# Optimization experiments

Measured on AMD Instinct MI355X. Metric: run time of the kernel, lower is better.

## Reference

```python
import jax, jax.numpy as jnp
import numpy as np

N = 30000      # input points
M = 7500       # sampled queries = floor(N * ratio), ratio=0.25
K = 16         # neighbors per query
D_X = 64       # input feature dim
D_REL = 64     # point_pos_nn output dim
D_F = D_X + D_REL  # fij_hat dim = 128


def setup_inputs() -> dict:
    key = jax.random.key(0)
    ks = jax.random.split(key, 6)
    x = jax.random.normal(ks[0], (N, D_X), jnp.float32)
    pos = jax.random.normal(ks[1], (N, 3), jnp.float32)
    idx = jax.random.randint(ks[2], (M,), 0, N)
    W_pos = jax.random.normal(ks[3], (10, D_REL), jnp.float32) / jnp.sqrt(10.0)
    b_pos = jnp.zeros((D_REL,), jnp.float32)
    W_att = jax.random.normal(ks[4], (D_F, D_F), jnp.float32) / jnp.sqrt(float(D_F))
    b_att = jnp.zeros((D_F,), jnp.float32)
    W_glob = jax.random.normal(ks[5], (D_F, D_F), jnp.float32) / jnp.sqrt(float(D_F))
    b_glob = jnp.zeros((D_F,), jnp.float32)
    return {"x": x, "pos": pos, "idx": idx, "W_pos": W_pos, "b_pos": b_pos,
            "W_att": W_att, "b_att": b_att, "W_glob": W_glob, "b_glob": b_glob}


def reference(x, pos, idx, W_pos, b_pos, W_att, b_att, W_glob, b_glob):
    # --- KNN: brute-force squared distances from sampled queries to all points ---
    pos_q = pos[idx]                                         # [M, 3]
    d2 = ((pos_q * pos_q).sum(-1)[:, None]
          + (pos * pos).sum(-1)[None, :]
          - 2.0 * pos_q @ pos.T)                             # [M, N]
    _, nbr = jax.lax.top_k(-d2, K)                           # [M, K] neighbor indices

    # --- Local Spatial Encoding (message) ---
    pos_j = pos[nbr]                                         # [M, K, 3]
    pos_i = jnp.broadcast_to(pos_q[:, None, :], pos_j.shape) # [M, K, 3]
    vij = pos_i - pos_j                                      # [M, K, 3]
    dij = jnp.linalg.norm(vij, axis=-1, keepdims=True)       # [M, K, 1]
    rel = jnp.concatenate([pos_i, pos_j, vij, dij], axis=-1) # [M, K, 10]
    rij = jax.nn.relu(rel @ W_pos + b_pos)                   # [M, K, D_REL]

    # --- Attentive pooling ---
    fij = jnp.concatenate([x[nbr], rij], axis=-1)            # [M, K, D_F]
    g = fij @ W_att + b_att                                  # [M, K, D_F]
    s = jax.nn.softmax(g, axis=-1)                           # softmax over feature dim
    aggr = jnp.mean(s * fij, axis=1)                         # mean over K neighbors -> [M, D_F]

    # --- global_nn (update) ---
    return jax.nn.relu(aggr @ W_glob + b_glob)               # [M, D_F]
```

## Files before the change

### kernel.cpp

```cpp
#include <hip/hip_runtime.h>
#include <stdint.h>

#define KQ     8
#define KNB    16
#define CAPC   256
#define CAPG   512
#define NCHUNK 4

typedef short short8 __attribute__((ext_vector_type(8)));
typedef float floatx4 __attribute__((ext_vector_type(4)));
typedef float floatx2 __attribute__((ext_vector_type(2)));

__device__ __forceinline__ unsigned short f2bf(float x) {
  union { float f; uint32_t u; } v; v.f = x;
  uint32_t u = v.u + 0x7FFFu + ((v.u >> 16) & 1u);
  return (unsigned short)(u >> 16);
}
__device__ __forceinline__ float bf2f(unsigned short b) {
  return __uint_as_float(((uint32_t)b) << 16);
}
__device__ __forceinline__ float rfl(float v) {
  return __int_as_float(__builtin_amdgcn_readfirstlane(__float_as_int(v)));
}

static __device__ __forceinline__ floatx2 fma2(floatx2 a, floatx2 b, floatx2 c) {
#if __has_builtin(__builtin_elementwise_fma)
  return __builtin_elementwise_fma(a, b, c);
#else
  floatx2 r; r[0] = fmaf(a[0], b[0], c[0]); r[1] = fmaf(a[1], b[1], c[1]);
  return r;
#endif
}
static __device__ __forceinline__ floatx2 min2(floatx2 a, floatx2 b) {
#if __has_builtin(__builtin_elementwise_min)
  return __builtin_elementwise_min(a, b);
#else
  floatx2 r; r[0] = fminf(a[0], b[0]); r[1] = fminf(a[1], b[1]);
  return r;
#endif
}
static __device__ __forceinline__ floatx2 sp2(float v) {
  floatx2 r; r[0] = v; r[1] = v; return r;
}

__global__ void prep_kernel(const float* __restrict__ pos,
                            const float* __restrict__ W_att,
                            float4* __restrict__ pos4,
                            float* __restrict__ pospk,
                            unsigned short* __restrict__ Wt,
                            int* __restrict__ cnt_g, int N, int Npad2, int M) {
  int id = blockIdx.x * 256 + threadIdx.x;
  if (id < Npad2) {
    int j = id;
    float px = 0.f, py = 0.f, pz = 0.f, pp = 3.0e38f;
    if (j < N) {
      px = pos[3 * j]; py = pos[3 * j + 1]; pz = pos[3 * j + 2];
      pp = fmaf(px, px, fmaf(py, py, pz * pz));
      pos4[j] = make_float4(px, py, pz, pp);
    }
    int pair = j >> 1, h = j & 1;
    float* dst = pospk + (size_t)pair * 8;
    dst[0 + h] = px; dst[2 + h] = py; dst[4 + h] = pz; dst[6 + h] = pp;
  } else if (id < Npad2 + 128 * 128) {
    int t = id - Npad2;
    int c = t >> 7, f = t & 127;
    Wt[f * 128 + c] = f2bf(W_att[t]);
  } else if (id < Npad2 + 128 * 128 + M) {
    cnt_g[id - Npad2 - 128 * 128] = 0;
  }
}

__global__ __launch_bounds__(256) void knn_kernel(
    const float4* __restrict__ pos4, const float4* __restrict__ pospk4,
    const int* __restrict__ idx, uint32_t* __restrict__ cand_g,
    int* __restrict__ cnt_g, int Npad2, int M) {
  __shared__ uint32_t cand[KQ][CAPC];
  __shared__ int cnt[KQ];
  __shared__ float gmin[KQ][16];
  __shared__ float tau_s[KQ];

  const int tid = threadIdx.x;
  const int wid = tid >> 6, lane = tid & 63;
  const int qg = blockIdx.x >> 2, chunk = blockIdx.x & 3;
  const int q0 = qg * KQ;
  const int iters = Npad2 >> 11;
  const int pbase = chunk * (Npad2 >> 3);
  const int jbase = chunk * (Npad2 >> 2);

  float sx[KQ], sy[KQ], sz[KQ];
#pragma unroll
  for (int qi = 0; qi < KQ; ++qi) {
    int m = q0 + qi; if (m >= M) m = M - 1;
    float4 qp = pos4[idx[m]];
    sx[qi] = rfl(-2.f * qp.x); sy[qi] = rfl(-2.f * qp.y);
    sz[qi] = rfl(-2.f * qp.z);
  }
  if (tid < KQ) cnt[tid] = 0;

  floatx2 tmn[KQ];
#pragma unroll
  for (int qi = 0; qi < KQ; ++qi) tmn[qi] = sp2(3.4e38f);
  {
    int pg = (pbase + tid) * 2;
    float4 a = pospk4[pg], b = pospk4[pg + 1];
    for (int it = 0; it < iters; ++it) {
      float4 an = a, bn = b;
      if (it + 1 < iters) {
        int pgn = (pbase + (it + 1) * 256 + tid) * 2;
        an = pospk4[pgn]; bn = pospk4[pgn + 1];
      }
      floatx2 X, Y, Z, W;
      X[0] = a.x; X[1] = a.y; Y[0] = a.z; Y[1] = a.w;
      Z[0] = b.x; Z[1] = b.y; W[0] = b.z; W[1] = b.w;
#pragma unroll
      for (int qi = 0; qi < KQ; ++qi) {
        floatx2 t = fma2(sp2(sx[qi]), X,
                         fma2(sp2(sy[qi]), Y, fma2(sp2(sz[qi]), Z, W)));
        tmn[qi] = min2(tmn[qi], t);
      }
      a = an; b = bn;
    }
  }
#pragma unroll
  for (int qi = 0; qi < KQ; ++qi) {
    float v = fminf(tmn[qi][0], tmn[qi][1]);
    v = fminf(v, __shfl_xor(v, 1));
    v = fminf(v, __shfl_xor(v, 2));
    v = fminf(v, __shfl_xor(v, 4));
    v = fminf(v, __shfl_xor(v, 8));
    if ((tid & 15) == 0) gmin[qi][tid >> 4] = v;
  }
  __syncthreads();
  if (tid < KQ) {
    float t = gmin[tid][0];
#pragma unroll
    for (int g = 1; g < 16; ++g) t = fmaxf(t, gmin[tid][g]);
    tau_s[tid] = t + fabsf(t) * 1e-6f + 1e-7f;
  }
  __syncthreads();
  float tau[KQ];
#pragma unroll
  for (int qi = 0; qi < KQ; ++qi) tau[qi] = rfl(tau_s[qi]);

  {
    int pg = (pbase + tid) * 2;
    float4 a = pospk4[pg], b = pospk4[pg + 1];
    for (int it = 0; it < iters; ++it) {
      float4 an = a, bn = b;
      if (it + 1 < iters) {
        int pgn = (pbase + (it + 1) * 256 + tid) * 2;
        an = pospk4[pgn]; bn = pospk4[pgn + 1];
      }
      floatx2 X, Y, Z, W;
      X[0] = a.x; X[1] = a.y; Y[0] = a.z; Y[1] = a.w;
      Z[0] = b.x; Z[1] = b.y; W[0] = b.z; W[1] = b.w;
      const int j0 = jbase + it * 512 + tid * 2;
#pragma unroll
      for (int qi = 0; qi < KQ; ++qi) {
        floatx2 t = fma2(sp2(sx[qi]), X,
                         fma2(sp2(sy[qi]), Y, fma2(sp2(sz[qi]), Z, W)));
        if (fminf(t[0], t[1]) <= tau[qi]) {
          if (t[0] <= tau[qi]) {
            int sl = atomicAdd(&cnt[qi], 1);
            if (sl < CAPC) cand[qi][sl] = (uint32_t)j0;
          }
          if (t[1] <= tau[qi]) {
            int sl = atomicAdd(&cnt[qi], 1);
            if (sl < CAPC) cand[qi][sl] = (uint32_t)(j0 + 1);
          }
        }
      }
      a = an; b = bn;
    }
  }
  __syncthreads();

#pragma unroll
  for (int i = 0; i < 2; ++i) {
    int qi = wid * 2 + i;
    int m = q0 + qi;
    if (m < M) {
      int nc = cnt[qi]; if (nc > CAPC) nc = CAPC;
      int base = 0;
      if (lane == 0) base = atomicAdd(&cnt_g[m], nc);
      base = __shfl(base, 0);
      for (int s = lane; s < nc; s += 64) {
        int p = base + s;
        if (p < CAPG) cand_g[(size_t)m * CAPG + p] = cand[qi][s];
      }
    }
  }
}

__global__ __launch_bounds__(256) void merge_kernel(
    const float4* __restrict__ pos4, const int* __restrict__ idx,
    const uint32_t* __restrict__ cand_g, const int* __restrict__ cnt_g,
    int* __restrict__ nbr, int M) {
  const int tid = threadIdx.x;
  const int lane = tid & 63;
  const int m = blockIdx.x * 4 + (tid >> 6);
  if (m >= M) return;

  float4 qp = pos4[idx[m]];
  int nc = cnt_g[m]; if (nc > CAPG) nc = CAPG;

  unsigned long long c[CAPG / 64];
#pragma unroll
  for (int ch = 0; ch < CAPG / 64; ++ch) {
    c[ch] = ~0ull;
    int s = ch * 64 + lane;
    if (s < nc) {
      uint32_t j = cand_g[(size_t)m * CAPG + s];
      float4 pj = pos4[j];
      float dot = fmaf(qp.x, pj.x, fmaf(qp.y, pj.y, qp.z * pj.z));
      float tt  = fmaf(-2.f, dot, pj.w);
      float d2  = fmaxf(qp.w + tt, 0.f);
      c[ch] = ((unsigned long long)__float_as_uint(d2) << 32) | j;
    }
  }
#pragma unroll
  for (int r = 0; r < KNB; ++r) {
    unsigned long long mn = c[0];
#pragma unroll
    for (int ch = 1; ch < CAPG / 64; ++ch) mn = (c[ch] < mn) ? c[ch] : mn;
#pragma unroll
    for (int off = 1; off < 64; off <<= 1) {
      unsigned long long o = __shfl_xor(mn, off);
      mn = (o < mn) ? o : mn;
    }
    if (lane == 0) nbr[m * KNB + r] = (int)(uint32_t)mn;
#pragma unroll
    for (int ch = 0; ch < CAPG / 64; ++ch)
      if (c[ch] == mn) c[ch] = ~0ull;
  }
}

__global__ __launch_bounds__(256) void mid_kernel(
    const float* __restrict__ x, const float4* __restrict__ pos4,
    const int* __restrict__ idx, const float* __restrict__ W_pos,
    const float* __restrict__ b_pos, const unsigned short* __restrict__ Wt,
    const float* __restrict__ b_att, const int* __restrict__ nbr,
    float* __restrict__ aggr, int M) {
  __shared__ __align__(16) unsigned short fijb[8][16][136];
  __shared__ int nbr_s[128];
  __shared__ float4 qpos_s[8];

  const int tid = threadIdx.x;
  const int wid = tid >> 6, lane = tid & 63;
  const int col = lane & 15, quad = lane >> 4;
  const int b = blockIdx.x;

  if (tid < 128) {
    int mq = b * 8 + (tid >> 4); if (mq >= M) mq = M - 1;
    nbr_s[tid] = nbr[mq * 16 + (tid & 15)];
  }
  if (tid < 8) {
    int mq = b * 8 + tid; if (mq >= M) mq = M - 1;
    qpos_s[tid] = pos4[idx[mq]];
  }
  float wp[10];
#pragma unroll
  for (int t = 0; t < 10; ++t) wp[t] = W_pos[t * 64 + lane];
  float bp = b_pos[lane];
  __syncthreads();

  {
    int rr = tid >> 1, h = tid & 1;
    int jn = nbr_s[rr];
    const float4* src = (const float4*)(x + (size_t)jn * 64) + h * 8;
    short8* dst = (short8*)&fijb[rr >> 4][rr & 15][h * 32];
#pragma unroll
    for (int i = 0; i < 4; ++i) {
      float4 u = src[2 * i], v = src[2 * i + 1];
      short8 w;
      w[0] = (short)f2bf(u.x); w[1] = (short)f2bf(u.y);
      w[2] = (short)f2bf(u.z); w[3] = (short)f2bf(u.w);
      w[4] = (short)f2bf(v.x); w[5] = (short)f2bf(v.y);
      w[6] = (short)f2bf(v.z); w[7] = (short)f2bf(v.w);
      dst[i] = w;
    }
  }
#pragma unroll
  for (int qi = 0; qi < 2; ++qi) {
    int q = wid * 2 + qi;
    float4 qp = qpos_s[q];
#pragma unroll 4
    for (int k = 0; k < 16; ++k) {
      int jn = nbr_s[q * 16 + k];
      float4 pj = pos4[jn];
      float vx = qp.x - pj.x, vy = qp.y - pj.y, vz = qp.z - pj.z;
      float dd = sqrtf(fmaf(vx, vx, fmaf(vy, vy, vz * vz)));
      float r = bp;
      r = fmaf(qp.x, wp[0], r); r = fmaf(qp.y, wp[1], r); r = fmaf(qp.z, wp[2], r);
      r = fmaf(pj.x, wp[3], r); r = fmaf(pj.y, wp[4], r); r = fmaf(pj.z, wp[5], r);
      r = fmaf(vx, wp[6], r);  r = fmaf(vy, wp[7], r);  r = fmaf(vz, wp[8], r);
      r = fmaf(dd, wp[9], r);
      r = fmaxf(r, 0.f);
      fijb[q][k][64 + lane] = f2bf(r);
    }
  }
  __syncthreads();

#pragma unroll 1
  for (int qi = 0; qi < 2; ++qi) {
    int q = wid * 2 + qi;
    int mq = b * 8 + q;

    short8 af[4];
#pragma unroll
    for (int cs = 0; cs < 4; ++cs)
      af[cs] = *(const short8*)&fijb[q][col][cs * 32 + quad * 8];

    floatx4 acc[8];
#pragma unroll
    for (int ft = 0; ft < 8; ++ft) {
      float bav = b_att[ft * 16 + col];
      floatx4 a = {bav, bav, bav, bav};
#pragma unroll
      for (int cs = 0; cs < 4; ++cs) {
        short8 bfrag =
            *(const short8*)&Wt[(ft * 16 + col) * 128 + cs * 32 + quad * 8];
        a = __builtin_amdgcn_mfma_f32_16x16x32_bf16(af[cs], bfrag, a, 0, 0, 0);
      }
      acc[ft] = a;
    }

    float rowmax[4], rowinv[4];
#pragma unroll
    for (int r = 0; r < 4; ++r) {
      float mx = acc[0][r];
#pragma unroll
      for (int ft = 1; ft < 8; ++ft) mx = fmaxf(mx, acc[ft][r]);
      mx = fmaxf(mx, __shfl_xor(mx, 1));
      mx = fmaxf(mx, __shfl_xor(mx, 2));
      mx = fmaxf(mx, __shfl_xor(mx, 4));
      mx = fmaxf(mx, __shfl_xor(mx, 8));
      float sm = 0.f;
#pragma unroll
      for (int ft = 0; ft < 8; ++ft) sm += __expf(acc[ft][r] - mx);
      sm += __shfl_xor(sm, 1);
      sm += __shfl_xor(sm, 2);
      sm += __shfl_xor(sm, 4);
      sm += __shfl_xor(sm, 8);
      rowmax[r] = mx;
      rowinv[r] = 1.0f / sm;
    }

#pragma unroll
    for (int ft = 0; ft < 8; ++ft) {
      float ap = 0.f;
#pragma unroll
      for (int r = 0; r < 4; ++r) {
        float s = __expf(acc[ft][r] - rowmax[r]) * rowinv[r];
        float fv = bf2f(fijb[q][quad * 4 + r][ft * 16 + col]);
        ap = fmaf(s, fv, ap);
      }
      ap += __shfl_xor(ap, 16);
      ap += __shfl_xor(ap, 32);
      if (quad == 0 && mq < M)
        aggr[mq * 128 + ft * 16 + col] = ap * (1.0f / 16.0f);
    }
  }
}

__global__ __launch_bounds__(256) void out_kernel(
    const float* __restrict__ aggr, const float* __restrict__ W_glob,
    const float* __restrict__ b_glob, float* __restrict__ out, int M) {
  __shared__ float ag[16][128];
  const int tid = threadIdx.x;
  const int mbase = blockIdx.x * 16;
  for (int s = tid; s < 16 * 128; s += 256) {
    int r = s >> 7, cc = s & 127;
    int m = mbase + r;
    ((float*)ag)[s] = (m < M) ? aggr[m * 128 + cc] : 0.0f;
  }
  __syncthreads();
  const int f = tid & 127, h = tid >> 7;
  float acc[8];
  float bg = b_glob[f];
#pragma unroll
  for (int i = 0; i < 8; ++i) acc[i] = bg;
  for (int c = 0; c < 128; c += 4) {
    float w0 = W_glob[(c + 0) * 128 + f];
    float w1 = W_glob[(c + 1) * 128 + f];
    float w2 = W_glob[(c + 2) * 128 + f];
    float w3 = W_glob[(c + 3) * 128 + f];
#pragma unroll
    for (int i = 0; i < 8; ++i) {
      const floatx4 a4 = *(const floatx4*)&ag[h * 8 + i][c];
      acc[i] += a4[0] * w0 + a4[1] * w1 + a4[2] * w2 + a4[3] * w3;
    }
  }
#pragma unroll
  for (int i = 0; i < 8; ++i) {
    int m = mbase + h * 8 + i;
    if (m < M) out[m * 128 + f] = fmaxf(acc[i], 0.0f);
  }
}

extern "C" void kernel_launch(void* const* d_in, const int* in_sizes, int n_in,
                              void* d_out, int out_size, void* d_ws,
                              size_t ws_size, hipStream_t stream) {
  const float* x      = (const float*)d_in[0];
  const float* pos    = (const float*)d_in[1];
  const int*   idx    = (const int*)d_in[2];
  const float* W_pos  = (const float*)d_in[3];
  const float* b_pos  = (const float*)d_in[4];
  const float* W_att  = (const float*)d_in[5];
  const float* b_att  = (const float*)d_in[6];
  const float* W_glob = (const float*)d_in[7];
  const float* b_glob = (const float*)d_in[8];
  float* out = (float*)d_out;

  const int N = in_sizes[1] / 3;
  const int M = in_sizes[2];
  const int Npad2 = (N + 2047) & ~2047;

  char* ws = (char*)d_ws;
  size_t o = 0;
  float4* pos4 = (float4*)(ws + o);               o += ((size_t)N * 16 + 255) & ~(size_t)255;
  float* pospk = (float*)(ws + o);                o += ((size_t)Npad2 * 16 + 255) & ~(size_t)255;
  unsigned short* Wt = (unsigned short*)(ws + o); o += (128 * 128 * 2 + 255) & ~(size_t)255;
  int* nbr = (int*)(ws + o);                      o += (((size_t)M * KNB * 4) + 255) & ~(size_t)255;
  uint32_t* cand_g = (uint32_t*)(ws + o);         o += (((size_t)M * CAPG * 4) + 255) & ~(size_t)255;
  int* cnt_g = (int*)(ws + o);                    o += (((size_t)M * 4) + 255) & ~(size_t)255;
  float* aggr = (float*)(ws + o);

  int prep_ids = Npad2 + 128 * 128 + M;
  prep_kernel<<<(prep_ids + 255) / 256, 256, 0, stream>>>(
      pos, W_att, pos4, pospk, Wt, cnt_g, N, Npad2, M);
  knn_kernel<<<((M + KQ - 1) / KQ) * NCHUNK, 256, 0, stream>>>(
      pos4, (const float4*)pospk, idx, cand_g, cnt_g, Npad2, M);
  merge_kernel<<<(M + 3) / 4, 256, 0, stream>>>(pos4, idx, cand_g, cnt_g, nbr,
                                                M);
  mid_kernel<<<(M + 7) / 8, 256, 0, stream>>>(x, pos4, idx, W_pos, b_pos, Wt,
                                              b_att, nbr, aggr, M);
  out_kernel<<<(M + 15) / 16, 256, 0, stream>>>(aggr, W_glob, b_glob, out, M);
}
```

Measured before the change: 242.5 us.

## Collapse pipeline into two kernels with per-chunk top-k and fused output GEMM

Removes the prep and merge kernels. The KNN kernel now reads raw pos directly, computes norms on the fly, converts W_att inside its first blocks, doubles queries per block to 16, and does a per-chunk top-16 selection in-block. It writes 64 packed candidates per query instead of a global candidate list with atomics. The mid and output kernels are merged, so the neighbour merge over 64 candidates and the W_glob projection run inside one fused kernel, avoiding the aggr round-trip and extra launches. The trade-off is stride-3 unpacked position loads, more registers for 16 queries, and a fused kernel that reads W_glob from global per block.

Result: slower. 418.4 us (+72.5%).

```diff
diff --git a/kernel.cpp b/kernel.cpp
--- a/kernel.cpp
+++ b/kernel.cpp
@@ -1,11 +1,10 @@
 #include <hip/hip_runtime.h>
 #include <stdint.h>
 
-#define KQ     8
+#define KQ     16
+#define NCHUNK 4
+#define CAPC   256
 #define KNB    16
-#define CAPC   256
-#define CAPG   512
-#define NCHUNK 4
 
 typedef short short8 __attribute__((ext_vector_type(8)));
 typedef float floatx4 __attribute__((ext_vector_type(4)));
@@ -43,57 +42,37 @@
   floatx2 r; r[0] = v; r[1] = v; return r;
 }
 
-__global__ void prep_kernel(const float* __restrict__ pos,
-                            const float* __restrict__ W_att,
-                            float4* __restrict__ pos4,
-                            float* __restrict__ pospk,
-                            unsigned short* __restrict__ Wt,
-                            int* __restrict__ cnt_g, int N, int Npad2, int M) {
-  int id = blockIdx.x * 256 + threadIdx.x;
-  if (id < Npad2) {
-    int j = id;
-    float px = 0.f, py = 0.f, pz = 0.f, pp = 3.0e38f;
-    if (j < N) {
-      px = pos[3 * j]; py = pos[3 * j + 1]; pz = pos[3 * j + 2];
-      pp = fmaf(px, px, fmaf(py, py, pz * pz));
-      pos4[j] = make_float4(px, py, pz, pp);
-    }
-    int pair = j >> 1, h = j & 1;
-    float* dst = pospk + (size_t)pair * 8;
-    dst[0 + h] = px; dst[2 + h] = py; dst[4 + h] = pz; dst[6 + h] = pp;
-  } else if (id < Npad2 + 128 * 128) {
-    int t = id - Npad2;
-    int c = t >> 7, f = t & 127;
-    Wt[f * 128 + c] = f2bf(W_att[t]);
-  } else if (id < Npad2 + 128 * 128 + M) {
-    cnt_g[id - Npad2 - 128 * 128] = 0;
-  }
-}
-
 __global__ __launch_bounds__(256) void knn_kernel(
-    const float4* __restrict__ pos4, const float4* __restrict__ pospk4,
-    const int* __restrict__ idx, uint32_t* __restrict__ cand_g,
-    int* __restrict__ cnt_g, int Npad2, int M) {
+    const float* __restrict__ pos, const float* __restrict__ W_att,
+    const int* __restrict__ idx, unsigned long long* __restrict__ cand_out,
+    unsigned short* __restrict__ Wt, int N, int Npad, int M) {
   __shared__ uint32_t cand[KQ][CAPC];
   __shared__ int cnt[KQ];
   __shared__ float gmin[KQ][16];
   __shared__ float tau_s[KQ];
 
   const int tid = threadIdx.x;
-  const int wid = tid >> 6, lane = tid & 63;
+  const int wv = tid >> 6, lane = tid & 63;
   const int qg = blockIdx.x >> 2, chunk = blockIdx.x & 3;
   const int q0 = qg * KQ;
-  const int iters = Npad2 >> 11;
-  const int pbase = chunk * (Npad2 >> 3);
-  const int jbase = chunk * (Npad2 >> 2);
-
-  float sx[KQ], sy[KQ], sz[KQ];
+  const int chunkPts = Npad >> 2;
+  const int iters = chunkPts >> 9;
+  const int jbase = chunk * chunkPts;
+
+  if (blockIdx.x < 64) {
+    int id = blockIdx.x * 256 + tid;
+    int c = id >> 7, f = id & 127;
+    Wt[f * 128 + c] = f2bf(W_att[id]);
+  }
+
+  float sx[KQ], sy[KQ], sz[KQ], qq[KQ];
 #pragma unroll
   for (int qi = 0; qi < KQ; ++qi) {
     int m = q0 + qi; if (m >= M) m = M - 1;
-    float4 qp = pos4[idx[m]];
-    sx[qi] = rfl(-2.f * qp.x); sy[qi] = rfl(-2.f * qp.y);
-    sz[qi] = rfl(-2.f * qp.z);
+    int ii = idx[m];
+    float ax = pos[3 * ii], ay = pos[3 * ii + 1], az = pos[3 * ii + 2];
+    sx[qi] = rfl(-2.f * ax); sy[qi] = rfl(-2.f * ay); sz[qi] = rfl(-2.f * az);
+    qq[qi] = rfl(fmaf(ax, ax, fmaf(ay, ay, az * az)));
   }
   if (tid < KQ) cnt[tid] = 0;
 
@@ -101,24 +80,27 @@
 #pragma unroll
   for (int qi = 0; qi < KQ; ++qi) tmn[qi] = sp2(3.4e38f);
   {
-    int pg = (pbase + tid) * 2;
-    float4 a = pospk4[pg], b = pospk4[pg + 1];
+    int j0 = jbase + tid;
+    int cA = (j0 < N) ? j0 : N - 1, cB = (j0 + 256 < N) ? j0 + 256 : N - 1;
+    float x0 = pos[3 * cA], y0 = pos[3 * cA + 1], z0 = pos[3 * cA + 2];
+    float x1 = pos[3 * cB], y1 = pos[3 * cB + 1], z1 = pos[3 * cB + 2];
     for (int it = 0; it < iters; ++it) {
-      float4 an = a, bn = b;
-      if (it + 1 < iters) {
-        int pgn = (pbase + (it + 1) * 256 + tid) * 2;
-        an = pospk4[pgn]; bn = pospk4[pgn + 1];
-      }
-      floatx2 X, Y, Z, W;
-      X[0] = a.x; X[1] = a.y; Y[0] = a.z; Y[1] = a.w;
-      Z[0] = b.x; Z[1] = b.y; W[0] = b.z; W[1] = b.w;
+      int jn = j0 + 512;
+      int nA = (jn < N) ? jn : N - 1, nB = (jn + 256 < N) ? jn + 256 : N - 1;
+      float nx0 = pos[3 * nA], ny0 = pos[3 * nA + 1], nz0 = pos[3 * nA + 2];
+      float nx1 = pos[3 * nB], ny1 = pos[3 * nB + 1], nz1 = pos[3 * nB + 2];
+      floatx2 X, Y, Z;
+      X[0] = x0; X[1] = x1; Y[0] = y0; Y[1] = y1; Z[0] = z0; Z[1] = z1;
+      floatx2 W = fma2(X, X, fma2(Y, Y, Z * Z));
+      W[0] = (j0 < N) ? W[0] : 3.0e38f;
+      W[1] = (j0 + 256 < N) ? W[1] : 3.0e38f;
 #pragma unroll
       for (int qi = 0; qi < KQ; ++qi) {
         floatx2 t = fma2(sp2(sx[qi]), X,
                          fma2(sp2(sy[qi]), Y, fma2(sp2(sz[qi]), Z, W)));
         tmn[qi] = min2(tmn[qi], t);
       }
-      a = an; b = bn;
+      x0 = nx0; y0 = ny0; z0 = nz0; x1 = nx1; y1 = ny1; z1 = nz1; j0 = jn;
     }
   }
 #pragma unroll
@@ -143,18 +125,20 @@
   for (int qi = 0; qi < KQ; ++qi) tau[qi] = rfl(tau_s[qi]);
 
   {
-    int pg = (pbase + tid) * 2;
-    float4 a = pospk4[pg], b = pospk4[pg + 1];
+    int j0 = jbase + tid;
+    int cA = (j0 < N) ? j0 : N - 1, cB = (j0 + 256 < N) ? j0 + 256 : N - 1;
+    float x0 = pos[3 * cA], y0 = pos[3 * cA + 1], z0 = pos[3 * cA + 2];
+    float x1 = pos[3 * cB], y1 = pos[3 * cB + 1], z1 = pos[3 * cB + 2];
     for (int it = 0; it < iters; ++it) {
-      float4 an = a, bn = b;
-      if (it + 1 < iters) {
-        int pgn = (pbase + (it + 1) * 256 + tid) * 2;
-        an = pospk4[pgn]; bn = pospk4[pgn + 1];
-      }
-      floatx2 X, Y, Z, W;
-      X[0] = a.x; X[1] = a.y; Y[0] = a.z; Y[1] = a.w;
-      Z[0] = b.x; Z[1] = b.y; W[0] = b.z; W[1] = b.w;
-      const int j0 = jbase + it * 512 + tid * 2;
+      int jn = j0 + 512;
+      int nA = (jn < N) ? jn : N - 1, nB = (jn + 256 < N) ? jn + 256 : N - 1;
+      float nx0 = pos[3 * nA], ny0 = pos[3 * nA + 1], nz0 = pos[3 * nA + 2];
+      float nx1 = pos[3 * nB], ny1 = pos[3 * nB + 1], nz1 = pos[3 * nB + 2];
+      floatx2 X, Y, Z;
+      X[0] = x0; X[1] = x1; Y[0] = y0; Y[1] = y1; Z[0] = z0; Z[1] = z1;
+      floatx2 W = fma2(X, X, fma2(Y, Y, Z * Z));
+      W[0] = (j0 < N) ? W[0] : 3.0e38f;
+      W[1] = (j0 + 256 < N) ? W[1] : 3.0e38f;
 #pragma unroll
       for (int qi = 0; qi < KQ; ++qi) {
         floatx2 t = fma2(sp2(sx[qi]), X,
@@ -166,97 +150,94 @@
           }
           if (t[1] <= tau[qi]) {
             int sl = atomicAdd(&cnt[qi], 1);
-            if (sl < CAPC) cand[qi][sl] = (uint32_t)(j0 + 1);
+            if (sl < CAPC) cand[qi][sl] = (uint32_t)(j0 + 256);
           }
         }
       }
-      a = an; b = bn;
-    }
-  }
-  __syncthreads();
-
-#pragma unroll
-  for (int i = 0; i < 2; ++i) {
-    int qi = wid * 2 + i;
+      x0 = nx0; y0 = ny0; z0 = nz0; x1 = nx1; y1 = ny1; z1 = nz1; j0 = jn;
+    }
+  }
+  __syncthreads();
+
+#pragma unroll
+  for (int i = 0; i < 4; ++i) {
+    int qi = wv * 4 + i;
     int m = q0 + qi;
-    if (m < M) {
-      int nc = cnt[qi]; if (nc > CAPC) nc = CAPC;
-      int base = 0;
-      if (lane == 0) base = atomicAdd(&cnt_g[m], nc);
-      base = __shfl(base, 0);
-      for (int s = lane; s < nc; s += 64) {
-        int p = base + s;
-        if (p < CAPG) cand_g[(size_t)m * CAPG + p] = cand[qi][s];
-      }
-    }
-  }
-}
-
-__global__ __launch_bounds__(256) void merge_kernel(
-    const float4* __restrict__ pos4, const int* __restrict__ idx,
-    const uint32_t* __restrict__ cand_g, const int* __restrict__ cnt_g,
-    int* __restrict__ nbr, int M) {
-  const int tid = threadIdx.x;
-  const int lane = tid & 63;
-  const int m = blockIdx.x * 4 + (tid >> 6);
-  if (m >= M) return;
-
-  float4 qp = pos4[idx[m]];
-  int nc = cnt_g[m]; if (nc > CAPG) nc = CAPG;
-
-  unsigned long long c[CAPG / 64];
-#pragma unroll
-  for (int ch = 0; ch < CAPG / 64; ++ch) {
-    c[ch] = ~0ull;
-    int s = ch * 64 + lane;
-    if (s < nc) {
-      uint32_t j = cand_g[(size_t)m * CAPG + s];
-      float4 pj = pos4[j];
-      float dot = fmaf(qp.x, pj.x, fmaf(qp.y, pj.y, qp.z * pj.z));
-      float tt  = fmaf(-2.f, dot, pj.w);
-      float d2  = fmaxf(qp.w + tt, 0.f);
-      c[ch] = ((unsigned long long)__float_as_uint(d2) << 32) | j;
-    }
-  }
-#pragma unroll
-  for (int r = 0; r < KNB; ++r) {
-    unsigned long long mn = c[0];
-#pragma unroll
-    for (int ch = 1; ch < CAPG / 64; ++ch) mn = (c[ch] < mn) ? c[ch] : mn;
-#pragma unroll
-    for (int off = 1; off < 64; off <<= 1) {
-      unsigned long long o = __shfl_xor(mn, off);
-      mn = (o < mn) ? o : mn;
-    }
-    if (lane == 0) nbr[m * KNB + r] = (int)(uint32_t)mn;
-#pragma unroll
-    for (int ch = 0; ch < CAPG / 64; ++ch)
-      if (c[ch] == mn) c[ch] = ~0ull;
-  }
-}
-
-__global__ __launch_bounds__(256) void mid_kernel(
-    const float* __restrict__ x, const float4* __restrict__ pos4,
+    int nc = cnt[qi]; if (nc > CAPC) nc = CAPC;
+    unsigned long long c[CAPC / 64];
+#pragma unroll
+    for (int ch = 0; ch < CAPC / 64; ++ch) {
+      c[ch] = ~0ull;
+      int s = ch * 64 + lane;
+      if (s < nc) {
+        uint32_t j = cand[qi][s];
+        float px = pos[3 * j], py = pos[3 * j + 1], pz = pos[3 * j + 2];
+        float pp = fmaf(px, px, fmaf(py, py, pz * pz));
+        float t = fmaf(sx[qi], px, fmaf(sy[qi], py, fmaf(sz[qi], pz, pp)));
+        float d2 = fmaxf(qq[qi] + t, 0.f);
+        c[ch] = ((unsigned long long)__float_as_uint(d2) << 32) | j;
+      }
+    }
+#pragma unroll
+    for (int r = 0; r < KNB; ++r) {
+      unsigned long long mn = c[0];
+#pragma unroll
+      for (int ch = 1; ch < CAPC / 64; ++ch) mn = (c[ch] < mn) ? c[ch] : mn;
+#pragma unroll
+      for (int off = 1; off < 64; off <<= 1) {
+        unsigned long long o = __shfl_xor(mn, off);
+        mn = (o < mn) ? o : mn;
+      }
+      if (m < M && lane == 0)
+        cand_out[(size_t)m * 64 + chunk * 16 + r] = mn;
+#pragma unroll
+      for (int ch = 0; ch < CAPC / 64; ++ch)
+        if (c[ch] == mn) c[ch] = ~0ull;
+    }
+  }
+}
+
+__global__ __launch_bounds__(256) void fused_kernel(
+    const float* __restrict__ x, const float* __restrict__ pos,
     const int* __restrict__ idx, const float* __restrict__ W_pos,
     const float* __restrict__ b_pos, const unsigned short* __restrict__ Wt,
-    const float* __restrict__ b_att, const int* __restrict__ nbr,
-    float* __restrict__ aggr, int M) {
+    const float* __restrict__ b_att, const float* __restrict__ W_glob,
+    const float* __restrict__ b_glob,
+    const unsigned long long* __restrict__ cand_out,
+    float* __restrict__ out, int M) {
   __shared__ __align__(16) unsigned short fijb[8][16][136];
   __shared__ int nbr_s[128];
-  __shared__ float4 qpos_s[8];
+  __shared__ float qx_s[8], qy_s[8], qz_s[8];
+  __shared__ float agg[8][128];
 
   const int tid = threadIdx.x;
   const int wid = tid >> 6, lane = tid & 63;
   const int col = lane & 15, quad = lane >> 4;
   const int b = blockIdx.x;
 
-  if (tid < 128) {
-    int mq = b * 8 + (tid >> 4); if (mq >= M) mq = M - 1;
-    nbr_s[tid] = nbr[mq * 16 + (tid & 15)];
-  }
   if (tid < 8) {
     int mq = b * 8 + tid; if (mq >= M) mq = M - 1;
-    qpos_s[tid] = pos4[idx[mq]];
+    int ii = idx[mq];
+    qx_s[tid] = pos[3 * ii]; qy_s[tid] = pos[3 * ii + 1];
+    qz_s[tid] = pos[3 * ii + 2];
+  }
+
+#pragma unroll
+  for (int i = 0; i < 2; ++i) {
+    int q = wid * 2 + i;
+    int mq = b * 8 + q; if (mq >= M) mq = M - 1;
+    unsigned long long v = cand_out[(size_t)mq * 64 + lane];
+#pragma unroll
+    for (int r = 0; r < KNB; ++r) {
+      unsigned long long mn = v;
+#pragma unroll
+      for (int off = 1; off < 64; off <<= 1) {
+        unsigned long long o = __shfl_xor(mn, off);
+        mn = (o < mn) ? o : mn;
+      }
+      if (lane == 0) nbr_s[q * 16 + r] = (int)(uint32_t)mn;
+      if (v == mn) v = ~0ull;
+    }
   }
   float wp[10];
 #pragma unroll
@@ -283,16 +264,16 @@
 #pragma unroll
   for (int qi = 0; qi < 2; ++qi) {
     int q = wid * 2 + qi;
-    float4 qp = qpos_s[q];
+    float qxv = qx_s[q], qyv = qy_s[q], qzv = qz_s[q];
 #pragma unroll 4
     for (int k = 0; k < 16; ++k) {
       int jn = nbr_s[q * 16 + k];
-      float4 pj = pos4[jn];
-      float vx = qp.x - pj.x, vy = qp.y - pj.y, vz = qp.z - pj.z;
+      float px = pos[3 * jn], py = pos[3 * jn + 1], pz = pos[3 * jn + 2];
+      float vx = qxv - px, vy = qyv - py, vz = qzv - pz;
       float dd = sqrtf(fmaf(vx, vx, fmaf(vy, vy, vz * vz)));
       float r = bp;
-      r = fmaf(qp.x, wp[0], r); r = fmaf(qp.y, wp[1], r); r = fmaf(qp.z, wp[2], r);
-      r = fmaf(pj.x, wp[3], r); r = fmaf(pj.y, wp[4], r); r = fmaf(pj.z, wp[5], r);
+      r = fmaf(qxv, wp[0], r); r = fmaf(qyv, wp[1], r); r = fmaf(qzv, wp[2], r);
+      r = fmaf(px, wp[3], r);  r = fmaf(py, wp[4], r);  r = fmaf(pz, wp[5], r);
       r = fmaf(vx, wp[6], r);  r = fmaf(vy, wp[7], r);  r = fmaf(vz, wp[8], r);
       r = fmaf(dd, wp[9], r);
       r = fmaxf(r, 0.f);
@@ -304,7 +285,6 @@
 #pragma unroll 1
   for (int qi = 0; qi < 2; ++qi) {
     int q = wid * 2 + qi;
-    int mq = b * 8 + q;
 
     short8 af[4];
 #pragma unroll
@@ -357,44 +337,40 @@
       }
       ap += __shfl_xor(ap, 16);
       ap += __shfl_xor(ap, 32);
-      if (quad == 0 && mq < M)
-        aggr[mq * 128 + ft * 16 + col] = ap * (1.0f / 16.0f);
-    }
-  }
-}
-
-__global__ __launch_bounds__(256) void out_kernel(
-    const float* __restrict__ aggr, const float* __restrict__ W_glob,
-    const float* __restrict__ b_glob, float* __restrict__ out, int M) {
-  __shared__ float ag[16][128];
-  const int tid = threadIdx.x;
-  const int mbase = blockIdx.x * 16;
-  for (int s = tid; s < 16 * 128; s += 256) {
-    int r = s >> 7, cc = s & 127;
-    int m = mbase + r;
-    ((float*)ag)[s] = (m < M) ? aggr[m * 128 + cc] : 0.0f;
-  }
-  __syncthreads();
-  const int f = tid & 127, h = tid >> 7;
-  float acc[8];
-  float bg = b_glob[f];
-#pragma unroll
-  for (int i = 0; i < 8; ++i) acc[i] = bg;
-  for (int c = 0; c < 128; c += 4) {
-    float w0 = W_glob[(c + 0) * 128 + f];
-    float w1 = W_glob[(c + 1) * 128 + f];
-    float w2 = W_glob[(c + 2) * 128 + f];
-    float w3 = W_glob[(c + 3) * 128 + f];
-#pragma unroll
-    for (int i = 0; i < 8; ++i) {
-      const floatx4 a4 = *(const floatx4*)&ag[h * 8 + i][c];
-      acc[i] += a4[0] * w0 + a4[1] * w1 + a4[2] * w2 + a4[3] * w3;
-    }
-  }
-#pragma unroll
-  for (int i = 0; i < 8; ++i) {
-    int m = mbase + h * 8 + i;
-    if (m < M) out[m * 128 + f] = fmaxf(acc[i], 0.0f);
+      if (quad == 0) agg[q][ft * 16 + col] = ap * (1.0f / 16.0f);
+    }
+  }
+  __syncthreads();
+
+  {
+    const int f = tid & 127, h = tid >> 7;
+    float a0[4], a1[4];
+#pragma unroll
+    for (int i = 0; i < 4; ++i) {
+      a0[i] = agg[h * 4 + i][lane];
+      a1[i] = agg[h * 4 + i][64 + lane];
+    }
+    float bg = b_glob[f];
+    float acc[4];
+#pragma unroll
+    for (int i = 0; i < 4; ++i) acc[i] = bg;
+#pragma unroll 16
+    for (int c = 0; c < 64; ++c) {
+      float w = W_glob[c * 128 + f];
+#pragma unroll
+      for (int i = 0; i < 4; ++i) acc[i] = fmaf(__shfl(a0[i], c), w, acc[i]);
+    }
+#pragma unroll 16
+    for (int c = 0; c < 64; ++c) {
+      float w = W_glob[(64 + c) * 128 + f];
+#pragma unroll
+      for (int i = 0; i < 4; ++i) acc[i] = fmaf(__shfl(a1[i], c), w, acc[i]);
+    }
+#pragma unroll
+    for (int i = 0; i < 4; ++i) {
+      int m = b * 8 + h * 4 + i;
+      if (m < M) out[m * 128 + f] = fmaxf(acc[i], 0.0f);
+    }
   }
 }
 
@@ -414,26 +390,18 @@
 
   const int N = in_sizes[1] / 3;
   const int M = in_sizes[2];
-  const int Npad2 = (N + 2047) & ~2047;
+  const int Npad = (N + 2047) & ~2047;
 
   char* ws = (char*)d_ws;
   size_t o = 0;
-  float4* pos4 = (float4*)(ws + o);               o += ((size_t)N * 16 + 255) & ~(size_t)255;
-  float* pospk = (float*)(ws + o);                o += ((size_t)Npad2 * 16 + 255) & ~(size_t)255;
-  unsigned short* Wt = (unsigned short*)(ws + o); o += (128 * 128 * 2 + 255) & ~(size_t)255;
-  int* nbr = (int*)(ws + o);                      o += (((size_t)M * KNB * 4) + 255) & ~(size_t)255;
-  uint32_t* cand_g = (uint32_t*)(ws + o);         o += (((size_t)M * CAPG * 4) + 255) & ~(size_t)255;
-  int* cnt_g = (int*)(ws + o);                    o += (((size_t)M * 4) + 255) & ~(size_t)255;
-  float* aggr = (float*)(ws + o);
-
-  int prep_ids = Npad2 + 128 * 128 + M;
-  prep_kernel<<<(prep_ids + 255) / 256, 256, 0, stream>>>(
-      pos, W_att, pos4, pospk, Wt, cnt_g, N, Npad2, M);
-  knn_kernel<<<((M + KQ - 1) / KQ) * NCHUNK, 256, 0, stream>>>(
-      pos4, (const float4*)pospk, idx, cand_g, cnt_g, Npad2, M);
-  merge_kernel<<<(M + 3) / 4, 256, 0, stream>>>(pos4, idx, cand_g, cnt_g, nbr,
-                                                M);
-  mid_kernel<<<(M + 7) / 8, 256, 0, stream>>>(x, pos4, idx, W_pos, b_pos, Wt,
-                                              b_att, nbr, aggr, M);
-  out_kernel<<<(M + 15) / 16, 256, 0, stream>>>(aggr, W_glob, b_glob, out, M);
-}
+  unsigned long long* cand_out = (unsigned long long*)(ws + o);
+  o += (((size_t)M * 64 * 8) + 255) & ~(size_t)255;
+  unsigned short* Wt = (unsigned short*)(ws + o);
+  o += (128 * 128 * 2 + 255) & ~(size_t)255;
+
+  const int QG = (M + KQ - 1) / KQ;
+  knn_kernel<<<QG * NCHUNK, 256, 0, stream>>>(pos, W_att, idx, cand_out, Wt,
+                                              N, Npad, M);
+  fused_kernel<<<(M + 7) / 8, 256, 0, stream>>>(
+      x, pos, idx, W_pos, b_pos, Wt, b_att, W_glob, b_glob, cand_out, out, M);
+}
```
